# Kernel optimization log

Hardware: AMD Instinct MI355X
Metric: run time of the kernel (lower is better)

## Reference

```python
import jax, jax.numpy as jnp
import numpy as np

B, C, L = 32, 512, 16          # batch, clauses per CNF, max literals per clause
D, H, P = 256, 1024, 16        # clause_hidden_dim, hidden_size, prefix_tokens
NH, NL = 8, 4                  # adapter_heads, adapter_layers
MAXV = 512                     # max_variables


def _ln(x, w, b, eps=1e-5):
    m = jnp.mean(x, axis=-1, keepdims=True)
    v = jnp.mean(jnp.square(x - m), axis=-1, keepdims=True)
    return (x - m) * jax.lax.rsqrt(v + eps) * w + b


def _mha(q, k, v, w_in, b_in, w_out, b_out, nh):
    E = q.shape[-1]
    dh = E // nh
    wq, wk, wv = jnp.split(w_in, 3, axis=0)
    bq, bk, bv = jnp.split(b_in, 3, axis=0)

    def heads(x, w, b):
        y = x @ w.T + b
        return y.reshape(x.shape[0], x.shape[1], nh, dh).transpose(0, 2, 1, 3)

    qh, kh, vh = heads(q, wq, bq), heads(k, wk, bk), heads(v, wv, bv)
    att = jax.nn.softmax(jnp.einsum('bhqd,bhkd->bhqk', qh, kh) * (1.0 / np.sqrt(dh)), axis=-1)
    o = jnp.einsum('bhqk,bhkd->bhqd', att, vh).transpose(0, 2, 1, 3).reshape(q.shape[0], q.shape[1], E)
    return o @ w_out.T + b_out


def setup_inputs() -> dict:
    key = jax.random.key(0)
    ks = jax.random.split(key, 16)
    s = 0.02
    var_idx = jax.random.randint(ks[0], (B, C, L), 0, MAXV + 1)
    sign_idx = jax.random.randint(ks[1], (B, C, L), 1, 3)   # 1=positive literal, 2=negative
    lens = jax.random.randint(ks[2], (B, C), 1, L + 1)      # ragged clause lengths >= 1
    lit_mask = jnp.arange(L)[None, None, :] < lens[..., None]
    inp = dict(var_idx=var_idx, sign_idx=sign_idx, lit_mask=lit_mask)
    inp['var_emb'] = jax.random.normal(ks[3], (MAXV + 1, D)) * s
    inp['sign_emb'] = jax.random.normal(ks[4], (3, D)) * s
    inp['litpos_emb'] = jax.random.normal(ks[5], (L, D)) * s
    inp['clausepos_emb'] = jax.random.normal(ks[6], (C, D)) * s
    inp['enc_in_w'] = jax.random.normal(ks[7], (NL, 3 * D, D)) * s
    inp['enc_in_b'] = jnp.zeros((NL, 3 * D))
    inp['enc_out_w'] = jax.random.normal(ks[8], (NL, D, D)) * s
    inp['enc_out_b'] = jnp.zeros((NL, D))
    inp['enc_ff1_w'] = jax.random.normal(ks[9], (NL, 4 * D, D)) * s
    inp['enc_ff1_b'] = jnp.zeros((NL, 4 * D))
    inp['enc_ff2_w'] = jax.random.normal(ks[10], (NL, D, 4 * D)) * s
    inp['enc_ff2_b'] = jnp.zeros((NL, D))
    inp['enc_n1_w'] = jnp.ones((NL, D))
    inp['enc_n1_b'] = jnp.zeros((NL, D))
    inp['enc_n2_w'] = jnp.ones((NL, D))
    inp['enc_n2_b'] = jnp.zeros((NL, D))
    inp['th_ln_w'] = jnp.ones((D,))
    inp['th_ln_b'] = jnp.zeros((D,))
    inp['th_w'] = jax.random.normal(ks[11], (H, D)) * s
    inp['th_b'] = jnp.zeros((H,))
    inp['pq'] = jax.random.normal(ks[12], (P, H))
    inp['pa_in_w'] = jax.random.normal(ks[13], (3 * H, H)) * s
    inp['pa_in_b'] = jnp.zeros((3 * H,))
    inp['pa_out_w'] = jax.random.normal(ks[14], (H, H)) * s
    inp['pa_out_b'] = jnp.zeros((H,))
    inp['pn_w'] = jnp.ones((H,))
    inp['pn_b'] = jnp.zeros((H,))
    return inp


def reference(var_idx, sign_idx, lit_mask, var_emb, sign_emb, litpos_emb, clausepos_emb,
              enc_in_w, enc_in_b, enc_out_w, enc_out_b, enc_ff1_w, enc_ff1_b,
              enc_ff2_w, enc_ff2_b, enc_n1_w, enc_n1_b, enc_n2_w, enc_n2_b,
              th_ln_w, th_ln_b, th_w, th_b, pq, pa_in_w, pa_in_b, pa_out_w, pa_out_b,
              pn_w, pn_b):
    # literal states [B,C,L,D]: four embedding gathers fused into one expression
    lit = (var_emb[var_idx] + sign_emb[sign_idx]
           + litpos_emb[None, None, :, :] + clausepos_emb[None, :, None, :])
    m = lit_mask[..., None].astype(lit.dtype)
    x = jnp.sum(lit * m, axis=2) / jnp.sum(m, axis=2)   # masked mean-pool -> [B,C,D]
    for i in range(NL):  # PyTorch post-norm TransformerEncoderLayer, gelu (exact)
        a = _mha(x, x, x, enc_in_w[i], enc_in_b[i], enc_out_w[i], enc_out_b[i], NH)
        x = _ln(x + a, enc_n1_w[i], enc_n1_b[i])
        f = jax.nn.gelu(x @ enc_ff1_w[i].T + enc_ff1_b[i], approximate=False) @ enc_ff2_w[i].T + enc_ff2_b[i]
        x = _ln(x + f, enc_n2_w[i], enc_n2_b[i])
    ch = _ln(x, th_ln_w, th_ln_b) @ th_w.T + th_b       # to_hidden -> [B,C,H]
    q = jnp.broadcast_to(pq[None], (ch.shape[0], P, H))
    pref = _mha(q, ch, ch, pa_in_w, pa_in_b, pa_out_w, pa_out_b, NH)
    return _ln(pref + q, pn_w, pn_b)                    # [B,P,H]
```

## Files before the change

### kernel.cpp

```cpp
#include <hip/hip_runtime.h>
#include <hip/hip_bf16.h>

typedef unsigned short u16;
typedef unsigned int u32;
typedef __attribute__((ext_vector_type(8))) short short8;
typedef __attribute__((ext_vector_type(4))) float floatx4;

#define BB 32
#define CC 512
#define LL 16
#define DD 256
#define HH 1024
#define PP 16
#define NLAY 4

__device__ __forceinline__ float bf2f(u16 u) {
  u32 x = ((u32)u) << 16; float f; __builtin_memcpy(&f, &x, 4); return f;
}
__device__ __forceinline__ u16 f2bf(float f) {
  __hip_bfloat16 h = __float2bfloat16(f);
  u16 r; __builtin_memcpy(&r, &h, 2); return r;
}
__device__ __forceinline__ void gload_lds16(const u16* g, u16* l) {
  __builtin_amdgcn_global_load_lds(
      (const __attribute__((address_space(1))) void*)g,
      (__attribute__((address_space(3))) void*)l, 16, 0, 0);
}

__global__ __launch_bounds__(256) void cvt_kernel(
    const float* __restrict__ s0, const float* __restrict__ s1,
    const float* __restrict__ s2, const float* __restrict__ s3,
    const float* __restrict__ s4, const float* __restrict__ s5,
    const float* __restrict__ s6, const float* __restrict__ s7,
    const float* __restrict__ s8, const float* __restrict__ s9,
    const float* __restrict__ s10, const float* __restrict__ s11,
    u16* __restrict__ dst)
{
  const float* srcs[12] = {s0, s1, s2, s3, s4, s5, s6, s7, s8, s9, s10, s11};
  const int pfx[12] = {786432, 1048576, 2097152, 3145728, 3407872, 6553600, 7602176,
                       7618560, 7749888, 7750656, 7754752, 7885824};
  int e = (blockIdx.x * 256 + threadIdx.x) * 4;
  int seg = 0;
  while (e >= pfx[seg]) seg++;
  int start = seg ? pfx[seg - 1] : 0;
  float4 f = *(const float4*)(srcs[seg] + (e - start));
  u16 o[4] = {f2bf(f.x), f2bf(f.y), f2bf(f.z), f2bf(f.w)};
  *(uint2*)(dst + e) = *(const uint2*)o;
}

__global__ __launch_bounds__(256) void thwT_kernel(
    const float* __restrict__ thw, u16* __restrict__ out)
{
  __shared__ float tile[32][33];
  int bx = blockIdx.x & 7, by = blockIdx.x >> 3;
  int tx = threadIdx.x & 31, ty = threadIdx.x >> 5;
  #pragma unroll
  for (int i = 0; i < 4; ++i) {
    int h = by * 32 + ty + i * 8, d = bx * 32 + tx;
    tile[ty + i * 8][tx] = thw[h * 256 + d];
  }
  __syncthreads();
  #pragma unroll
  for (int i = 0; i < 4; ++i) {
    int d = bx * 32 + ty + i * 8, h = by * 32 + tx;
    out[d * 1024 + h] = f2bf(tile[tx][ty + i * 8]);
  }
}

__global__ __launch_bounds__(256) void biasfold_kernel(
    const u16* __restrict__ Wkv, const float* __restrict__ thb,
    const float* __restrict__ paib, float* __restrict__ out)
{
  int wv = threadIdx.x >> 6, lane = threadIdx.x & 63;
  int n = blockIdx.x * 4 + wv;
  const u16* wr = Wkv + (size_t)n * 1024;
  float s = 0.f;
  #pragma unroll
  for (int i = 0; i < 16; ++i) {
    int h = i * 64 + lane;
    s += bf2f(wr[h]) * thb[h];
  }
  #pragma unroll
  for (int off = 32; off; off >>= 1) s += __shfl_xor(s, off);
  if (!lane) out[n] = s + paib[1024 + n];
}

__global__ __launch_bounds__(256) void redk_kernel(
    const float* __restrict__ part, const float* __restrict__ bias,
    const float* __restrict__ res, float* __restrict__ outf, u16* __restrict__ outb,
    int N, int nz, int total, int flags)
{
  int idx = (blockIdx.x * 256 + threadIdx.x) * 4;
  if (idx >= total) return;
  float4 a = *(const float4*)(part + idx);
  for (int z = 1; z < nz; ++z) {
    float4 b = *(const float4*)(part + (size_t)z * total + idx);
    a.x += b.x; a.y += b.y; a.z += b.z; a.w += b.w;
  }
  int row = idx / N, col = idx - row * N;
  float v4[4] = {a.x, a.y, a.z, a.w};
  #pragma unroll
  for (int i = 0; i < 4; ++i) {
    if (bias) v4[i] += bias[col + i];
    if (res) v4[i] += res[(size_t)((flags & 4) ? (row & 15) : row) * N + col + i];
  }
  if (outf) {
    *(float4*)(outf + idx) = *(const float4*)v4;
  } else {
    u16 o[4] = {f2bf(v4[0]), f2bf(v4[1]), f2bf(v4[2]), f2bf(v4[3])};
    *(uint2*)(outb + idx) = *(const uint2*)o;
  }
}

__global__ __launch_bounds__(256) void embed_kernel(
    const int* __restrict__ vi, const int* __restrict__ si, const int* __restrict__ mk,
    const u16* __restrict__ veb, const u16* __restrict__ seb,
    const u16* __restrict__ lpeb, const u16* __restrict__ cpeb,
    u16* __restrict__ xb)
{
  int t = threadIdx.x;
  int bc = blockIdx.x * 2 + (t >> 7);
  int c = bc & (CC - 1);
  int dl = (t & 127) * 2;
  int base = bc * LL;
  float a0 = 0.f, a1 = 0.f; int cnt = 0;
  #pragma unroll
  for (int l = 0; l < LL; ++l) {
    if (mk[base + l]) {
      int v = vi[base + l], s = si[base + l];
      u32 vv = *(const u32*)&veb[v * DD + dl];
      u32 sv = *(const u32*)&seb[s * DD + dl];
      u32 lv = *(const u32*)&lpeb[l * DD + dl];
      a0 += bf2f((u16)vv) + bf2f((u16)sv) + bf2f((u16)lv);
      a1 += bf2f((u16)(vv >> 16)) + bf2f((u16)(sv >> 16)) + bf2f((u16)(lv >> 16));
      cnt++;
    }
  }
  u32 cv = *(const u32*)&cpeb[c * DD + dl];
  float inv = 1.f / (float)cnt;
  u32 pk = (u32)f2bf(a0 * inv + bf2f((u16)cv)) | ((u32)f2bf(a1 * inv + bf2f((u16)(cv >> 16))) << 16);
  *(u32*)&xb[(size_t)bc * DD + dl] = pk;
}

template<int NC, bool GELU, bool LN, bool DLN>
__global__ __launch_bounds__(256) void gwide_kernel(
    const u16* __restrict__ A, const u16* __restrict__ W, const float* __restrict__ bias,
    const u16* __restrict__ resb, const float* __restrict__ gam, const float* __restrict__ bet,
    const float* __restrict__ gam2, const float* __restrict__ bet2,
    u16* __restrict__ out, int N, int K)
{
  constexpr int NT = NC / 32;
  __shared__ __align__(16) u16 As[32 * 64];
  __shared__ __align__(16) u16 Ws[NC * 64];
  __shared__ float sred[32][2][2];
  __shared__ float sred2[32][2][2];
  int t = threadIdx.x, lane = t & 63, w = t >> 6;
  int wm = w & 1, wn = w >> 1;
  int mrow = lane & 15, quad = lane >> 4;
  int bn0 = blockIdx.x * NC, bm0 = blockIdx.y * 32;

  int rA = t >> 3, gcA = (t & 7) ^ (rA & 7);
  const u16* gAp = A + (size_t)(bm0 + rA) * K + gcA * 8;
  u16* lAp = As + (w * 64) * 8;
  const u16* gW0 = W + (size_t)(bn0 + rA) * K + gcA * 8;
  u16* lW0 = Ws + (w * 64) * 8;

  floatx4 acc[NT];
  #pragma unroll
  for (int nt = 0; nt < NT; ++nt) acc[nt] = (floatx4){0.f, 0.f, 0.f, 0.f};

  for (int k0 = 0; k0 < K; k0 += 64) {
    __syncthreads();
    gload_lds16(gAp, lAp); gAp += 64;
    #pragma unroll
    for (int i = 0; i < NT; ++i)
      gload_lds16(gW0 + (size_t)i * 32 * K, lW0 + i * 2048);
    gW0 += 64;
    __syncthreads();
    #pragma unroll
    for (int ks = 0; ks < 2; ++ks) {
      int sw = ((ks * 4 + quad) ^ (mrow & 7)) * 8;
      short8 af = *(const short8*)&As[(wm * 16 + mrow) * 64 + sw];
      #pragma unroll
      for (int nt = 0; nt < NT; ++nt) {
        int rw = wn * (NC / 2) + nt * 16 + mrow;
        short8 bf = *(const short8*)&Ws[rw * 64 + sw];
        acc[nt] = __builtin_amdgcn_mfma_f32_16x16x32_bf16(af, bf, acc[nt], 0, 0, 0);
      }
    }
  }

  if constexpr (LN) {
    float val[NT][4];
    float bv[NT];
    #pragma unroll
    for (int nt = 0; nt < NT; ++nt) bv[nt] = bias[wn * 128 + nt * 16 + mrow];
    #pragma unroll
    for (int r = 0; r < 4; ++r) {
      int gm = bm0 + wm * 16 + quad * 4 + r;
      float sr = 0.f, s2r = 0.f;
      #pragma unroll
      for (int nt = 0; nt < NT; ++nt) {
        int gn = wn * 128 + nt * 16 + mrow;
        float v = acc[nt][r] + bv[nt] + bf2f(resb[(size_t)gm * 256 + gn]);
        val[nt][r] = v; sr += v; s2r += v * v;
      }
      sr += __shfl_xor(sr, 1); s2r += __shfl_xor(s2r, 1);
      sr += __shfl_xor(sr, 2); s2r += __shfl_xor(s2r, 2);
      sr += __shfl_xor(sr, 4); s2r += __shfl_xor(s2r, 4);
      sr += __shfl_xor(sr, 8); s2r += __shfl_xor(s2r, 8);
      if (mrow == 0) { sred[wm * 16 + quad * 4 + r][wn][0] = sr; sred[wm * 16 + quad * 4 + r][wn][1] = s2r; }
    }
    __syncthreads();
    #pragma unroll
    for (int r = 0; r < 4; ++r) {
      int lrow = wm * 16 + quad * 4 + r;
      float S = sred[lrow][0][0] + sred[lrow][1][0];
      float S2 = sred[lrow][0][1] + sred[lrow][1][1];
      float mean = S * (1.f / 256.f);
      float var = S2 * (1.f / 256.f) - mean * mean;
      float inv = rsqrtf(var + 1e-5f);
      float sr2 = 0.f, s2r2 = 0.f;
      #pragma unroll
      for (int nt = 0; nt < NT; ++nt) {
        int gn = wn * 128 + nt * 16 + mrow;
        float y = (val[nt][r] - mean) * inv * gam[gn] + bet[gn];
        val[nt][r] = y;
        if constexpr (DLN) { sr2 += y; s2r2 += y * y; }
        else out[(size_t)(bm0 + lrow) * 256 + gn] = f2bf(y);
      }
      if constexpr (DLN) {
        sr2 += __shfl_xor(sr2, 1); s2r2 += __shfl_xor(s2r2, 1);
        sr2 += __shfl_xor(sr2, 2); s2r2 += __shfl_xor(s2r2, 2);
        sr2 += __shfl_xor(sr2, 4); s2r2 += __shfl_xor(s2r2, 4);
        sr2 += __shfl_xor(sr2, 8); s2r2 += __shfl_xor(s2r2, 8);
        if (mrow == 0) { sred2[lrow][wn][0] = sr2; sred2[lrow][wn][1] = s2r2; }
      }
    }
    if constexpr (DLN) {
      __syncthreads();
      #pragma unroll
      for (int r = 0; r < 4; ++r) {
        int lrow = wm * 16 + quad * 4 + r;
        float S = sred2[lrow][0][0] + sred2[lrow][1][0];
        float S2 = sred2[lrow][0][1] + sred2[lrow][1][1];
        float mean = S * (1.f / 256.f);
        float var = S2 * (1.f / 256.f) - mean * mean;
        float inv = rsqrtf(var + 1e-5f);
        #pragma unroll
        for (int nt = 0; nt < NT; ++nt) {
          int gn = wn * 128 + nt * 16 + mrow;
          float z = (val[nt][r] - mean) * inv * gam2[gn] + bet2[gn];
          out[(size_t)(bm0 + lrow) * 256 + gn] = f2bf(z);
        }
      }
    }
  } else {
    #pragma unroll
    for (int nt = 0; nt < NT; ++nt) {
      int gn = bn0 + wn * (NC / 2) + nt * 16 + mrow;
      float bv = bias[gn];
      #pragma unroll
      for (int r = 0; r < 4; ++r) {
        int gm = bm0 + wm * 16 + quad * 4 + r;
        float v = acc[nt][r] + bv;
        if (GELU) v = 0.5f * v * (1.f + erff(v * 0.70710678118654752f));
        out[(size_t)gm * N + gn] = f2bf(v);
      }
    }
  }
}

__global__ __launch_bounds__(256) void gemm128s_kernel(
    const u16* __restrict__ A, const u16* __restrict__ W, const float* __restrict__ bias,
    u16* __restrict__ kb, u16* __restrict__ vtp,
    const u16* __restrict__ pqA, const u16* __restrict__ Wq, const float* __restrict__ biasq,
    u16* __restrict__ qh, int K)
{
  __shared__ __align__(16) u16 SH[16384];
  u16* As = SH;
  u16* Bs = SH + 8192;
  int t = threadIdx.x, lane = t & 63, w = t >> 6;
  int wm = w & 1, wn = w >> 1;
  int mrow = lane & 15, quad = lane >> 4;
  int id = blockIdx.x;
  int c, bm0, bn0;
  const u16* Abase; const u16* Wbase;
  int KK;
  if (id < 8) {
    c = -1; bm0 = 0; bn0 = id * 128;
    Abase = pqA; Wbase = Wq;
    KK = 1024;
  } else {
    int id2 = id - 8;
    int g = id2 >> 6, w6 = id2 & 63;
    int r4 = (w6 & 7) >> 1;
    c = ((w6 >> 3) << 1) | (w6 & 1);
    bm0 = (g * 4 + r4) * 128;
    bn0 = c * 128;
    Abase = A; Wbase = W;
    KK = K;
  }

  const u16* gA[4]; const u16* gB[4];
  u16* lA[4]; u16* lB[4];
  #pragma unroll
  for (int it = 0; it < 4; ++it) {
    int cc = w * 256 + it * 64 + lane;
    int r = cc >> 3;
    int gc = (cc & 7) ^ (r & 7);
    gA[it] = Abase + (size_t)(bm0 + r) * KK + gc * 8;
    gB[it] = Wbase + (size_t)(bn0 + r) * KK + gc * 8;
    lA[it] = As + (w * 256 + it * 64) * 8;
    lB[it] = Bs + (w * 256 + it * 64) * 8;
  }
  floatx4 acc[4][4];
  #pragma unroll
  for (int i = 0; i < 4; ++i)
    #pragma unroll
    for (int j = 0; j < 4; ++j)
      acc[i][j] = (floatx4){0.f, 0.f, 0.f, 0.f};
  int sw0 = ((0 * 4 + quad) ^ (mrow & 7)) * 8;
  int sw1 = ((1 * 4 + quad) ^ (mrow & 7)) * 8;

  for (int k0 = 0; k0 < KK; k0 += 64) {
    __syncthreads();
    #pragma unroll
    for (int it = 0; it < 4; ++it) { gload_lds16(gA[it], lA[it]); gA[it] += 64; }
    #pragma unroll
    for (int it = 0; it < 4; ++it) { gload_lds16(gB[it], lB[it]); gB[it] += 64; }
    __syncthreads();
    #pragma unroll
    for (int ks = 0; ks < 2; ++ks) {
      int sw = ks ? sw1 : sw0;
      short8 af[4], bfr[4];
      #pragma unroll
      for (int mi = 0; mi < 4; ++mi)
        af[mi] = *(const short8*)&As[(wm * 64 + mi * 16 + mrow) * 64 + sw];
      #pragma unroll
      for (int nj = 0; nj < 4; ++nj)
        bfr[nj] = *(const short8*)&Bs[(wn * 64 + nj * 16 + mrow) * 64 + sw];
      #pragma unroll
      for (int mi = 0; mi < 4; ++mi)
        #pragma unroll
        for (int nj = 0; nj < 4; ++nj)
          acc[mi][nj] = __builtin_amdgcn_mfma_f32_16x16x32_bf16(af[mi], bfr[nj], acc[mi][nj], 0, 0, 0);
    }
  }

  if (c == -1) {
    if (wm == 0) {
      #pragma unroll
      for (int nj = 0; nj < 4; ++nj) {
        int gn = bn0 + wn * 64 + nj * 16 + mrow;
        float bv = biasq[gn];
        #pragma unroll
        for (int r = 0; r < 4; ++r) {
          int gm = quad * 4 + r;
          qh[(size_t)gm * 1024 + gn] = f2bf(acc[0][nj][r] + bv);
        }
      }
    }
  } else if (c < 8) {
    #pragma unroll
    for (int nj = 0; nj < 4; ++nj) {
      int gn = bn0 + wn * 64 + nj * 16 + mrow;
      float bv = bias[gn];
      #pragma unroll
      for (int mi = 0; mi < 4; ++mi)
        #pragma unroll
        for (int r = 0; r < 4; ++r) {
          int gm = bm0 + wm * 64 + mi * 16 + quad * 4 + r;
          kb[(size_t)gm * 1024 + gn] = f2bf(acc[mi][nj][r] + bv);
        }
    }
  } else {
    int h = c - 8;
    int b = bm0 >> 9, jt = (bm0 >> 7) & 3;
    size_t basev = ((size_t)(b * 8 + h) * 128) * 512 + jt * 128;
    #pragma unroll
    for (int pass = 0; pass < 2; ++pass) {
      __syncthreads();
      if (wn == pass) {
        #pragma unroll
        for (int nj = 0; nj < 4; ++nj) {
          int dl = nj * 16 + mrow;
          float bv = bias[bn0 + pass * 64 + dl];
          #pragma unroll
          for (int mi = 0; mi < 4; ++mi) {
            int jp = quad * 32 + wm * 4 + mi;
            #pragma unroll
            for (int r = 0; r < 4; ++r)
              SH[dl * 136 + jp + r * 8] = f2bf(acc[mi][nj][r] + bv);
          }
        }
      }
      __syncthreads();
      #pragma unroll
      for (int i = 0; i < 4; ++i) {
        int idx = t + i * 256;
        int d = idx >> 4, jc4 = (idx & 15) * 8;
        uint4 v = *(const uint4*)&SH[d * 136 + jc4];
        *(uint4*)(vtp + basev + (size_t)(pass * 64 + d) * 512 + jc4) = v;
      }
    }
  }
}

__global__ __launch_bounds__(256) void gemm128_kernel(
    const u16* __restrict__ A, const u16* __restrict__ W, const float* __restrict__ bias,
    const float* __restrict__ res, void* __restrict__ out,
    int M, int N, int K, int flags)
{
  __shared__ __align__(16) u16 As[128 * 64];
  __shared__ __align__(16) u16 Bs[128 * 64];
  int t = threadIdx.x;
  int lane = t & 63, w = t >> 6;
  int wm = w & 1, wn = w >> 1;
  int bn0 = blockIdx.x * 128, bm0 = blockIdx.y * 128;
  int mrow = lane & 15, quad = lane >> 4;
  int z = blockIdx.z, NZ = gridDim.z;
  int Kc = K / NZ, kbase = z * Kc;

  const u16* gA[4]; const u16* gB[4];
  u16* lA[4]; u16* lB[4];
  #pragma unroll
  for (int it = 0; it < 4; ++it) {
    int c = w * 256 + it * 64 + lane;
    int r = c >> 3;
    int gc = (c & 7) ^ (r & 7);
    gA[it] = A + (size_t)(bm0 + r) * K + kbase + gc * 8;
    gB[it] = W + (size_t)(bn0 + r) * K + kbase + gc * 8;
    lA[it] = As + (w * 256 + it * 64) * 8;
    lB[it] = Bs + (w * 256 + it * 64) * 8;
  }
  floatx4 acc[4][4];
  #pragma unroll
  for (int i = 0; i < 4; ++i)
    #pragma unroll
    for (int j = 0; j < 4; ++j)
      acc[i][j] = (floatx4){0.f, 0.f, 0.f, 0.f};
  int sw0 = ((0 * 4 + quad) ^ (mrow & 7)) * 8;
  int sw1 = ((1 * 4 + quad) ^ (mrow & 7)) * 8;

  for (int k0 = 0; k0 < Kc; k0 += 64) {
    __syncthreads();
    #pragma unroll
    for (int it = 0; it < 4; ++it) { gload_lds16(gA[it], lA[it]); gA[it] += 64; }
    #pragma unroll
    for (int it = 0; it < 4; ++it) { gload_lds16(gB[it], lB[it]); gB[it] += 64; }
    __syncthreads();
    #pragma unroll
    for (int ks = 0; ks < 2; ++ks) {
      int sw = ks ? sw1 : sw0;
      short8 af[4], bfr[4];
      #pragma unroll
      for (int mi = 0; mi < 4; ++mi)
        af[mi] = *(const short8*)&As[(wm * 64 + mi * 16 + mrow) * 64 + sw];
      #pragma unroll
      for (int nj = 0; nj < 4; ++nj)
        bfr[nj] = *(const short8*)&Bs[(wn * 64 + nj * 16 + mrow) * 64 + sw];
      #pragma unroll
      for (int mi = 0; mi < 4; ++mi)
        #pragma unroll
        for (int nj = 0; nj < 4; ++nj)
          acc[mi][nj] = __builtin_amdgcn_mfma_f32_16x16x32_bf16(af[mi], bfr[nj], acc[mi][nj], 0, 0, 0);
    }
  }
  if (NZ > 1) {
    float* po = (float*)out + (size_t)z * M * N;
    #pragma unroll
    for (int nj = 0; nj < 4; ++nj) {
      int gn = bn0 + wn * 64 + nj * 16 + mrow;
      #pragma unroll
      for (int mi = 0; mi < 4; ++mi)
        #pragma unroll
        for (int r = 0; r < 4; ++r) {
          int gm = bm0 + wm * 64 + mi * 16 + quad * 4 + r;
          po[(size_t)gm * N + gn] = acc[mi][nj][r];
        }
    }
    return;
  }
  bool do_gelu = (flags & 1) != 0, of32 = (flags & 2) != 0;
  #pragma unroll
  for (int nj = 0; nj < 4; ++nj) {
    int gn = bn0 + wn * 64 + nj * 16 + mrow;
    float bv = bias ? bias[gn] : 0.f;
    #pragma unroll
    for (int mi = 0; mi < 4; ++mi) {
      #pragma unroll
      for (int r = 0; r < 4; ++r) {
        int gm = bm0 + wm * 64 + mi * 16 + quad * 4 + r;
        float v = acc[mi][nj][r] + bv;
        if (do_gelu) v = 0.5f * v * (1.f + erff(v * 0.70710678118654752f));
        if (flags & 4) v += res[(size_t)(gm & 15) * N + gn];
        else if (res) v += res[(size_t)gm * N + gn];
        if (of32) ((float*)out)[(size_t)gm * N + gn] = v;
        else      ((u16*)out)[(size_t)gm * N + gn] = f2bf(v);
      }
    }
  }
}

template<int D>
__global__ __launch_bounds__(256) void lnw_kernel(
    const float* __restrict__ in, const float* __restrict__ w, const float* __restrict__ b,
    float* __restrict__ outf, u16* __restrict__ outb)
{
  constexpr int NV = D / 64;
  int lane = threadIdx.x & 63, wv = threadIdx.x >> 6;
  int row = blockIdx.x * 4 + wv;
  const float* xr = in + (size_t)row * D;
  float v[NV];
  float s = 0.f, s2 = 0.f;
  #pragma unroll
  for (int i = 0; i < NV; ++i) {
    v[i] = xr[lane + i * 64];
    s += v[i]; s2 += v[i] * v[i];
  }
  #pragma unroll
  for (int off = 32; off > 0; off >>= 1) { s += __shfl_xor(s, off); s2 += __shfl_xor(s2, off); }
  float mean = s / (float)D;
  float var = s2 / (float)D - mean * mean;
  float inv = rsqrtf(var + 1e-5f);
  #pragma unroll
  for (int i = 0; i < NV; ++i) {
    int col = lane + i * 64;
    float y = (v[i] - mean) * inv * w[col] + b[col];
    size_t o = (size_t)row * D + col;
    if (outf) outf[o] = y;
    if (outb) outb[o] = f2bf(y);
  }
}

__global__ __launch_bounds__(256, 5) void attn_enc5_kernel(
    const u16* __restrict__ qkv, u16* __restrict__ out)
{
  __shared__ __align__(16) u16 Ks[64 * 40];
  __shared__ __align__(16) u16 Vt[32 * 72];
  __shared__ __align__(16) u16 Pl[4 * 32 * 72];
  int qt = blockIdx.x, h = blockIdx.y, b = blockIdx.z;
  int t = threadIdx.x, lane = t & 63, w = t >> 6;
  int mrow = lane & 15, quad = lane >> 4;
  int q0 = qt * 128 + w * 32;
  short8 qf[2];
  #pragma unroll
  for (int mi = 0; mi < 2; ++mi)
    qf[mi] = *(const short8*)(qkv + (size_t)(b * CC + q0 + mi * 16 + mrow) * 768 + h * 32 + quad * 8);
  floatx4 o[2][2];
  #pragma unroll
  for (int mi = 0; mi < 2; ++mi)
    #pragma unroll
    for (int di = 0; di < 2; ++di) o[mi][di] = (floatx4){0.f, 0.f, 0.f, 0.f};
  float lst[2][4] = {{0.f,0.f,0.f,0.f},{0.f,0.f,0.f,0.f}};
  const float sc = 0.17677669529663687f * 1.4426950408889634f;
  const floatx4 zf = (floatx4){0.f, 0.f, 0.f, 0.f};
  for (int jt = 0; jt < 8; ++jt) {
    if (jt) __syncthreads();
    {
      int j = t >> 2, q4 = (t & 3) * 8;
      uint4 kk = *(const uint4*)(qkv + (size_t)(b * CC + jt * 64 + j) * 768 + 256 + h * 32 + q4);
      *(uint4*)&Ks[j * 40 + q4] = kk;
      uint4 vv = *(const uint4*)(qkv + (size_t)(b * CC + jt * 64 + j) * 768 + 512 + h * 32 + q4);
      u16 tmp[8]; *(uint4*)tmp = vv;
      int jp = (j & 15) * 4 + (j >> 4);
      #pragma unroll
      for (int i = 0; i < 8; ++i) Vt[(q4 + i) * 72 + jp] = tmp[i];
    }
    __syncthreads();
    floatx4 s[2][4];
    #pragma unroll
    for (int nj = 0; nj < 4; ++nj) {
      short8 bf = *(const short8*)&Ks[(nj * 16 + mrow) * 40 + quad * 8];
      s[0][nj] = __builtin_amdgcn_mfma_f32_16x16x32_bf16(qf[0], bf, zf, 0, 0, 0);
      s[1][nj] = __builtin_amdgcn_mfma_f32_16x16x32_bf16(qf[1], bf, zf, 0, 0, 0);
    }
    #pragma unroll
    for (int mi = 0; mi < 2; ++mi) {
      #pragma unroll
      for (int r = 0; r < 4; ++r) {
        float ps = 0.f; u16 hv[4];
        #pragma unroll
        for (int nj = 0; nj < 4; ++nj) {
          float p = exp2f(s[mi][nj][r] * sc);
          ps += p; hv[nj] = f2bf(p);
        }
        lst[mi][r] += ps;
        *(uint2*)&Pl[(w * 32 + mi * 16 + quad * 4 + r) * 72 + mrow * 4] = *(uint2*)hv;
      }
    }
    #pragma unroll
    for (int ks = 0; ks < 2; ++ks) {
      short8 a0 = *(const short8*)&Pl[(w * 32 + mrow) * 72 + ks * 32 + quad * 8];
      short8 a1 = *(const short8*)&Pl[(w * 32 + 16 + mrow) * 72 + ks * 32 + quad * 8];
      short8 b0 = *(const short8*)&Vt[mrow * 72 + ks * 32 + quad * 8];
      short8 b1 = *(const short8*)&Vt[(16 + mrow) * 72 + ks * 32 + quad * 8];
      o[0][0] = __builtin_amdgcn_mfma_f32_16x16x32_bf16(a0, b0, o[0][0], 0, 0, 0);
      o[0][1] = __builtin_amdgcn_mfma_f32_16x16x32_bf16(a0, b1, o[0][1], 0, 0, 0);
      o[1][0] = __builtin_amdgcn_mfma_f32_16x16x32_bf16(a1, b0, o[1][0], 0, 0, 0);
      o[1][1] = __builtin_amdgcn_mfma_f32_16x16x32_bf16(a1, b1, o[1][1], 0, 0, 0);
    }
  }
  #pragma unroll
  for (int mi = 0; mi < 2; ++mi) {
    #pragma unroll
    for (int r = 0; r < 4; ++r) {
      float l = lst[mi][r];
      l += __shfl_xor(l, 1); l += __shfl_xor(l, 2);
      l += __shfl_xor(l, 4); l += __shfl_xor(l, 8);
      float inv = 1.f / l;
      int row = b * CC + q0 + mi * 16 + quad * 4 + r;
      #pragma unroll
      for (int di = 0; di < 2; ++di)
        out[(size_t)row * DD + h * 32 + di * 16 + mrow] = f2bf(o[mi][di][r] * inv);
    }
  }
}

__global__ __launch_bounds__(256) void attn_pref2_kernel(
    const u16* __restrict__ qh, const u16* __restrict__ kb, const u16* __restrict__ vtp,
    u16* __restrict__ out)
{
  __shared__ __align__(16) u16 Pl[4 * 16 * 136];
  __shared__ float Ored[4 * 16 * 128];
  __shared__ float Lred[4 * 16];
  int h = blockIdx.x, b = blockIdx.y;
  int t = threadIdx.x, lane = t & 63, w = t >> 6;
  int mrow = lane & 15, quad = lane >> 4;
  const float sc = 0.08838834764831845f * 1.4426950408889634f;
  const floatx4 zf = (floatx4){0.f, 0.f, 0.f, 0.f};
  short8 qf[4];
  #pragma unroll
  for (int ks = 0; ks < 4; ++ks)
    qf[ks] = *(const short8*)(qh + mrow * HH + h * 128 + ks * 32 + quad * 8);
  const u16* kbase = kb + ((size_t)(b * CC + w * 128)) * 1024 + h * 128;
  floatx4 s[8];
  #pragma unroll
  for (int nj = 0; nj < 8; ++nj) {
    floatx4 a = zf;
    #pragma unroll
    for (int ks = 0; ks < 4; ++ks) {
      short8 kf = *(const short8*)(kbase + (size_t)(nj * 16 + mrow) * 1024 + ks * 32 + quad * 8);
      a = __builtin_amdgcn_mfma_f32_16x16x32_bf16(qf[ks], kf, a, 0, 0, 0);
    }
    s[nj] = a;
  }
  #pragma unroll
  for (int r = 0; r < 4; ++r) {
    float ps = 0.f; u16 hv[8];
    #pragma unroll
    for (int nj = 0; nj < 8; ++nj) {
      float p = exp2f(s[nj][r] * sc);
      ps += p; hv[nj] = f2bf(p);
    }
    ps += __shfl_xor(ps, 1); ps += __shfl_xor(ps, 2);
    ps += __shfl_xor(ps, 4); ps += __shfl_xor(ps, 8);
    if (mrow == 0) Lred[w * 16 + quad * 4 + r] = ps;
    *(uint4*)&Pl[(w * 16 + quad * 4 + r) * 136 + mrow * 8] = *(uint4*)hv;
  }
  short8 pa[4];
  #pragma unroll
  for (int ks = 0; ks < 4; ++ks)
    pa[ks] = *(const short8*)&Pl[(w * 16 + mrow) * 136 + ks * 32 + quad * 8];
  const u16* vbase = vtp + ((size_t)(b * 8 + h) * 128) * 512 + w * 128;
  floatx4 o[8];
  #pragma unroll
  for (int nd = 0; nd < 8; ++nd) o[nd] = zf;
  #pragma unroll
  for (int nd = 0; nd < 8; ++nd) {
    #pragma unroll
    for (int ks = 0; ks < 4; ++ks) {
      short8 vf = *(const short8*)(vbase + (size_t)(nd * 16 + mrow) * 512 + ks * 32 + quad * 8);
      o[nd] = __builtin_amdgcn_mfma_f32_16x16x32_bf16(pa[ks], vf, o[nd], 0, 0, 0);
    }
  }
  #pragma unroll
  for (int nd = 0; nd < 8; ++nd)
    #pragma unroll
    for (int r = 0; r < 4; ++r)
      Ored[(w * 16 + quad * 4 + r) * 128 + nd * 16 + mrow] = o[nd][r];
  __syncthreads();
  int row = t >> 4, d0 = (t & 15) * 8;
  float l = Lred[row] + Lred[16 + row] + Lred[32 + row] + Lred[48 + row];
  float inv = 1.f / l;
  u16 ov[8];
  #pragma unroll
  for (int i = 0; i < 8; ++i) {
    int d = d0 + i;
    float sum = Ored[row * 128 + d] + Ored[(16 + row) * 128 + d]
              + Ored[(32 + row) * 128 + d] + Ored[(48 + row) * 128 + d];
    ov[i] = f2bf(sum * inv);
  }
  *(uint4*)(out + ((size_t)(b * PP + row)) * HH + h * 128 + d0) = *(const uint4*)ov;
}

extern "C" void kernel_launch(void* const* d_in, const int* in_sizes, int n_in,
                              void* d_out, int out_size, void* d_ws, size_t ws_size,
                              hipStream_t stream)
{
  const int* vi = (const int*)d_in[0];
  const int* si = (const int*)d_in[1];
  const int* mk = (const int*)d_in[2];
  const float* ve   = (const float*)d_in[3];
  const float* se   = (const float*)d_in[4];
  const float* lpe  = (const float*)d_in[5];
  const float* cpe  = (const float*)d_in[6];
  const float* eiw  = (const float*)d_in[7];
  const float* eib  = (const float*)d_in[8];
  const float* eow  = (const float*)d_in[9];
  const float* eob  = (const float*)d_in[10];
  const float* f1w  = (const float*)d_in[11];
  const float* f1b  = (const float*)d_in[12];
  const float* f2w  = (const float*)d_in[13];
  const float* f2b  = (const float*)d_in[14];
  const float* n1w  = (const float*)d_in[15];
  const float* n1b  = (const float*)d_in[16];
  const float* n2w  = (const float*)d_in[17];
  const float* n2b  = (const float*)d_in[18];
  const float* tlw  = (const float*)d_in[19];
  const float* tlb  = (const float*)d_in[20];
  const float* thw  = (const float*)d_in[21];
  const float* thb  = (const float*)d_in[22];
  const float* pq   = (const float*)d_in[23];
  const float* paiw = (const float*)d_in[24];
  const float* paib = (const float*)d_in[25];
  const float* paow = (const float*)d_in[26];
  const float* paob = (const float*)d_in[27];
  const float* pnw  = (const float*)d_in[28];
  const float* pnb  = (const float*)d_in[29];

  const int NROW = BB * CC;
  const size_t MB = 1048576;
  char* base = (char*)d_ws;
  u16* xb   = (u16*)(base);
  u16* qkvb = (u16*)(base + 8 * MB);
  u16* atto = (u16*)(base + 32 * MB);
  u16* h1   = (u16*)(base + 8 * MB);
  u16* tln  = (u16*)(base + 96 * MB);
  u16* kb   = (u16*)(base);
  u16* vtp  = (u16*)(base + 32 * MB);
  u16* wcb   = (u16*)(base + 64 * MB);
  u16* thwTb = (u16*)(base + 65 * MB);
  float* bkv = (float*)(base + 66 * MB);
  float* skpart = (float*)(base + 80 * MB);
  u16* wbf  = (u16*)(base + 104 * MB);
  u16* qh    = (u16*)(base + 120 * MB);
  u16* prefo = qh + 32768;
  float* prefout = (float*)(base + 122 * MB);

  u16* eiw_b  = wbf + 0;
  u16* eow_b  = wbf + 786432;
  u16* f1w_b  = wbf + 1048576;
  u16* f2w_b  = wbf + 2097152;
  u16* thw_b  = wbf + 3145728;
  u16* paiw_b = wbf + 3407872;
  u16* paow_b = wbf + 6553600;
  u16* pqb    = wbf + 7602176;
  u16* veb    = wbf + 7618560;
  u16* seb    = wbf + 7749888;
  u16* lpeb   = wbf + 7750656;
  u16* cpeb   = wbf + 7754752;

  dim3 blk(256);
  cvt_kernel<<<7701, blk, 0, stream>>>(eiw, eow, f1w, f2w, thw, paiw, paow, pq,
                                       ve, se, lpe, cpe, wbf);
  thwT_kernel<<<256, blk, 0, stream>>>(thw, thwTb);
  biasfold_kernel<<<512, blk, 0, stream>>>(paiw_b + (size_t)HH * HH, thb, paib, bkv);
  gemm128_kernel<<<dim3(2, 16, 4), blk, 0, stream>>>(
      paiw_b + (size_t)HH * HH, thwTb, nullptr, nullptr, skpart, 2048, 256, HH, 0);
  redk_kernel<<<512, blk, 0, stream>>>(skpart, nullptr, nullptr, nullptr, wcb,
                                       256, 4, 2048 * 256, 0);
  embed_kernel<<<NROW/2, blk, 0, stream>>>(vi, si, mk, veb, seb, lpeb, cpeb, xb);
  for (int i = 0; i < NLAY; ++i) {
    gwide_kernel<384, false, false, false><<<dim3(2, NROW/32), blk, 0, stream>>>(
        xb, eiw_b + (size_t)i*768*DD, eib + i*768, nullptr, nullptr, nullptr, nullptr, nullptr,
        qkvb, 768, DD);
    attn_enc5_kernel<<<dim3(4, 8, BB), blk, 0, stream>>>(qkvb, atto);
    gwide_kernel<256, false, true, false><<<dim3(1, NROW/32), blk, 0, stream>>>(
        atto, eow_b + (size_t)i*DD*DD, eob + i*DD, xb, n1w + i*DD, n1b + i*DD, nullptr, nullptr,
        xb, DD, DD);
    gwide_kernel<256, true, false, false><<<dim3(4, NROW/32), blk, 0, stream>>>(
        xb, f1w_b + (size_t)i*HH*DD, f1b + i*HH, nullptr, nullptr, nullptr, nullptr, nullptr,
        h1, HH, DD);
    if (i < NLAY - 1) {
      gwide_kernel<256, false, true, false><<<dim3(1, NROW/32), blk, 0, stream>>>(
          h1, f2w_b + (size_t)i*DD*HH, f2b + i*DD, xb, n2w + i*DD, n2b + i*DD, nullptr, nullptr,
          xb, DD, HH);
    } else {
      gwide_kernel<256, false, true, true><<<dim3(1, NROW/32), blk, 0, stream>>>(
          h1, f2w_b + (size_t)i*DD*HH, f2b + i*DD, xb, n2w + i*DD, n2b + i*DD, tlw, tlb,
          tln, DD, HH);
    }
  }
  gemm128s_kernel<<<2056, blk, 0, stream>>>(
      tln, wcb, bkv, kb, vtp,
      pqb, paiw_b, paib, qh, DD);
  attn_pref2_kernel<<<dim3(8, BB), blk, 0, stream>>>(qh, kb, vtp, prefo);
  gemm128_kernel<<<dim3(1024/128, (BB*PP)/128, 4), blk, 0, stream>>>(
      prefo, paow_b, nullptr, nullptr, skpart, BB*PP, HH, HH, 0);
  redk_kernel<<<512, blk, 0, stream>>>(skpart, paob, pq, prefout, nullptr,
                                       1024, 4, BB*PP*HH, 4);
  lnw_kernel<1024><<<(BB*PP)/4, blk, 0, stream>>>(prefout, pnw, pnb, (float*)d_out, nullptr);
}
```

Baseline: 681.0 us.

## Use 128x128 tiled GEMM for QKV/FFN and split residual LayerNorm into separate kernel

The QKV projection and both FFN GEMMs now run on the 128x128-tile gemm128 kernel instead of the 32-row-wide gwide kernel, which gives more operand reuse per tile. Because the FF2 GEMM no longer fuses residual add and LayerNorm, a new lnres_kernel does residual+LN (plus the to_hidden LN on the last layer) in a separate pass, one wavefront per row. This trades an extra bf16 round trip of the FF2 output and an added launch for the higher GEMM efficiency. The LN also now rounds the FF2 output to bf16 before adding the residual, so numerics shift slightly.

```diff
diff --git a/kernel.cpp b/kernel.cpp
--- a/kernel.cpp
+++ b/kernel.cpp
@@ -269,6 +269,56 @@
       }
     }
   }
+}
+
+template<bool DLN>
+__global__ __launch_bounds__(256) void lnres_kernel(
+    const u16* __restrict__ f, const u16* __restrict__ res,
+    const float* __restrict__ gam, const float* __restrict__ bet,
+    const float* __restrict__ gam2, const float* __restrict__ bet2,
+    u16* __restrict__ out)
+{
+  int lane = threadIdx.x & 63, wv = threadIdx.x >> 6;
+  int row = blockIdx.x * 4 + wv;
+  size_t base = (size_t)row * 256 + lane * 4;
+  uint2 fv = *(const uint2*)(f + base);
+  uint2 rv = *(const uint2*)(res + base);
+  u16 fa[4], ra[4];
+  *(uint2*)fa = fv; *(uint2*)ra = rv;
+  float v[4];
+  float s = 0.f, s2 = 0.f;
+  #pragma unroll
+  for (int i = 0; i < 4; ++i) {
+    v[i] = bf2f(fa[i]) + bf2f(ra[i]);
+    s += v[i]; s2 += v[i] * v[i];
+  }
+  #pragma unroll
+  for (int off = 32; off > 0; off >>= 1) { s += __shfl_xor(s, off); s2 += __shfl_xor(s2, off); }
+  float mean = s * (1.f / 256.f);
+  float var = s2 * (1.f / 256.f) - mean * mean;
+  float inv = rsqrtf(var + 1e-5f);
+  float y[4];
+  float sy = 0.f, sy2 = 0.f;
+  #pragma unroll
+  for (int i = 0; i < 4; ++i) {
+    int col = lane * 4 + i;
+    y[i] = (v[i] - mean) * inv * gam[col] + bet[col];
+    if (DLN) { sy += y[i]; sy2 += y[i] * y[i]; }
+  }
+  if constexpr (DLN) {
+    #pragma unroll
+    for (int off = 32; off > 0; off >>= 1) { sy += __shfl_xor(sy, off); sy2 += __shfl_xor(sy2, off); }
+    float m2 = sy * (1.f / 256.f);
+    float v2 = sy2 * (1.f / 256.f) - m2 * m2;
+    float i2 = rsqrtf(v2 + 1e-5f);
+    #pragma unroll
+    for (int i = 0; i < 4; ++i) {
+      int col = lane * 4 + i;
+      y[i] = (y[i] - m2) * i2 * gam2[col] + bet2[col];
+    }
+  }
+  u16 o[4] = {f2bf(y[0]), f2bf(y[1]), f2bf(y[2]), f2bf(y[3])};
+  *(uint2*)(out + base) = *(const uint2*)o;
 }
 
 __global__ __launch_bounds__(256) void gemm128s_kernel(
@@ -737,6 +787,7 @@
   u16* qkvb = (u16*)(base + 8 * MB);
   u16* atto = (u16*)(base + 32 * MB);
   u16* h1   = (u16*)(base + 8 * MB);
+  u16* f2o  = (u16*)(base + 48 * MB);
   u16* tln  = (u16*)(base + 96 * MB);
   u16* kb   = (u16*)(base);
   u16* vtp  = (u16*)(base + 32 * MB);
@@ -773,24 +824,22 @@
                                        256, 4, 2048 * 256, 0);
   embed_kernel<<<NROW/2, blk, 0, stream>>>(vi, si, mk, veb, seb, lpeb, cpeb, xb);
   for (int i = 0; i < NLAY; ++i) {
-    gwide_kernel<384, false, false, false><<<dim3(2, NROW/32), blk, 0, stream>>>(
-        xb, eiw_b + (size_t)i*768*DD, eib + i*768, nullptr, nullptr, nullptr, nullptr, nullptr,
-        qkvb, 768, DD);
+    gemm128_kernel<<<dim3(6, NROW/128), blk, 0, stream>>>(
+        xb, eiw_b + (size_t)i*768*DD, eib + i*768, nullptr, qkvb, NROW, 768, DD, 0);
     attn_enc5_kernel<<<dim3(4, 8, BB), blk, 0, stream>>>(qkvb, atto);
     gwide_kernel<256, false, true, false><<<dim3(1, NROW/32), blk, 0, stream>>>(
         atto, eow_b + (size_t)i*DD*DD, eob + i*DD, xb, n1w + i*DD, n1b + i*DD, nullptr, nullptr,
         xb, DD, DD);
-    gwide_kernel<256, true, false, false><<<dim3(4, NROW/32), blk, 0, stream>>>(
-        xb, f1w_b + (size_t)i*HH*DD, f1b + i*HH, nullptr, nullptr, nullptr, nullptr, nullptr,
-        h1, HH, DD);
+    gemm128_kernel<<<dim3(8, NROW/128), blk, 0, stream>>>(
+        xb, f1w_b + (size_t)i*HH*DD, f1b + i*HH, nullptr, h1, NROW, HH, DD, 1);
+    gemm128_kernel<<<dim3(2, NROW/128), blk, 0, stream>>>(
+        h1, f2w_b + (size_t)i*DD*HH, f2b + i*DD, nullptr, f2o, NROW, DD, HH, 0);
     if (i < NLAY - 1) {
-      gwide_kernel<256, false, true, false><<<dim3(1, NROW/32), blk, 0, stream>>>(
-          h1, f2w_b + (size_t)i*DD*HH, f2b + i*DD, xb, n2w + i*DD, n2b + i*DD, nullptr, nullptr,
-          xb, DD, HH);
+      lnres_kernel<false><<<NROW/4, blk, 0, stream>>>(
+          f2o, xb, n2w + i*DD, n2b + i*DD, nullptr, nullptr, xb);
     } else {
-      gwide_kernel<256, false, true, true><<<dim3(1, NROW/32), blk, 0, stream>>>(
-          h1, f2w_b + (size_t)i*DD*HH, f2b + i*DD, xb, n2w + i*DD, n2b + i*DD, tlw, tlb,
-          tln, DD, HH);
+      lnres_kernel<true><<<NROW/4, blk, 0, stream>>>(
+          f2o, xb, n2w + i*DD, n2b + i*DD, tlw, tlb, tln);
     }
   }
   gemm128s_kernel<<<2056, blk, 0, stream>>>(
```

New measurement: 885.2 us. 1.3x slower.
